# Optimization experiments

Hardware: AMD Instinct MI355X
Metric: run time of the kernel (lower is better)

## Reference

```python
import jax, jax.numpy as jnp
import numpy as np

POOL_NUM = 1024
NEIGHBOR_NUM = 16


def setup_inputs() -> dict:
    key = jax.random.key(0)
    k1, k2 = jax.random.split(key)
    vertices = jax.random.normal(k1, (8, 4096, 3), dtype=jnp.float32)
    feature_map = jax.random.normal(k2, (8, 4096, 256), dtype=jnp.float32)
    return {"vertices": vertices, "feature_map": feature_map}


def _get_neighbor_index(vertices, neighbor_num):
    # vertices: (bs, N, 3) -> neighbor_index: (bs, N, neighbor_num)
    inner = jnp.einsum('bnd,bmd->bnm', vertices, vertices)  # (bs, N, N)
    quadratic = jnp.sum(vertices ** 2, axis=2)              # (bs, N)
    distance = -2.0 * inner + quadratic[:, None, :] + quadratic[:, :, None]
    # smallest k+1 distances -> top_k on negated distance
    _, idx = jax.lax.top_k(-distance, neighbor_num + 1)     # (bs, N, k+1)
    return idx[:, :, 1:]                                    # drop self


def reference(vertices, feature_map):
    bs, vertice_num, _ = vertices.shape
    neighbor_index = _get_neighbor_index(vertices, NEIGHBOR_NUM)  # (bs, N, k)
    # gather neighbor features: (bs, N, k, C)
    id_0 = jnp.arange(bs)[:, None, None]
    neighbor_feature = feature_map[id_0, neighbor_index]
    pooled_feature = jnp.max(neighbor_feature, axis=2)            # (bs, N, C)
    # deterministic random subsample of vertices (torch uses randperm)
    sample_idx = jax.random.permutation(jax.random.key(42), vertice_num)[:POOL_NUM]
    vertices_pool = vertices[:, sample_idx, :]                    # (bs, P, 3)
    feature_map_pool = pooled_feature[:, sample_idx, :]           # (bs, P, C)
    return (vertices_pool, feature_map_pool)
```

## Files before the change

### kernel.cpp

```cpp
#include <hip/hip_runtime.h>
#include <stdint.h>
#include <string.h>
#include <algorithm>

#define NV 4096
#define NPOOL 1024
#define NB 8
#define KNB 16
#define REMOVED 0xFFFFFFFFu
#define HIDX(b) ((((b) >> 4) | (((b) & 15) << 6)))

struct SIdx { unsigned short v[NPOOL]; };

static inline void tf2x32_host(uint32_t k0, uint32_t k1,
                               uint32_t c0, uint32_t c1,
                               uint32_t& o0, uint32_t& o1) {
  uint32_t ks0 = k0, ks1 = k1, ks2 = k0 ^ k1 ^ 0x1BD11BDAu;
  uint32_t x0 = c0 + ks0, x1 = c1 + ks1;
#define TFR(r) { x0 += x1; x1 = (x1 << (r)) | (x1 >> (32 - (r))); x1 ^= x0; }
  TFR(13) TFR(15) TFR(26) TFR(6)
  x0 += ks1; x1 += ks2 + 1u;
  TFR(17) TFR(29) TFR(16) TFR(24)
  x0 += ks2; x1 += ks0 + 2u;
  TFR(13) TFR(15) TFR(26) TFR(6)
  x0 += ks0; x1 += ks1 + 3u;
  TFR(17) TFR(29) TFR(16) TFR(24)
  x0 += ks1; x1 += ks2 + 4u;
  TFR(13) TFR(15) TFR(26) TFR(6)
  x0 += ks2; x1 += ks0 + 5u;
#undef TFR
  o0 = x0; o1 = x1;
}

static void compute_sample_idx(SIdx& out) {
  static_assert(sizeof(SIdx) == 2048, "kernarg size");
  uint64_t arr[NV];
  uint16_t x[NV], tmp[NV];
  for (int i = 0; i < NV; ++i) x[i] = (uint16_t)i;
  uint32_t kh = 0u, kl = 42u;
  for (int round = 0; round < 2; ++round) {
    uint32_t nkh, nkl, sh, sl, t0, t1;
    tf2x32_host(kh, kl, 0u, 0u, nkh, nkl);
    tf2x32_host(kh, kl, 0u, 1u, sh, sl);
    kh = nkh; kl = nkl;
    for (int i = 0; i < NV; ++i) {
      tf2x32_host(sh, sl, 0u, (uint32_t)i, t0, t1);
      arr[i] = ((uint64_t)(t0 ^ t1) << 32) | (uint32_t)i;
    }
    std::sort(arr, arr + NV);
    for (int i = 0; i < NV; ++i) tmp[i] = x[(uint32_t)(arr[i] & 0xffffffffu)];
    memcpy(x, tmp, sizeof(x));
  }
  for (int i = 0; i < NPOOL; ++i) out.v[i] = x[i];
}

#define FALLBACK(D, TAUB, WIN)                                             \
  {                                                                        \
    uint32_t mask = 0;                                                     \
    for (int r = 0; r < KNB; ++r) {                                        \
      uint32_t bv = REMOVED, bm = 0xFFFFFFFFu;                             \
      _Pragma("unroll")                                                    \
      for (int t = 0; t < 16; ++t) {                                       \
        const uint32_t v = (((mask >> t) & 1u) || ((D[t] >> 22) > (TAUB))) \
                               ? REMOVED : D[t];                           \
        const uint32_t m = (uint32_t)((tid << 4) + t);                     \
        if (v < bv || (v == bv && m < bm)) { bv = v; bm = m; }             \
      }                                                                    \
      for (int off = 32; off > 0; off >>= 1) {                             \
        const uint32_t ov = (uint32_t)__shfl_down((int)bv, off);           \
        const uint32_t om = (uint32_t)__shfl_down((int)bm, off);           \
        if (ov < bv || (ov == bv && om < bm)) { bv = ov; bm = om; }        \
      }                                                                    \
      if (lane == 0) wmin[warp] = ((unsigned long long)bv << 32) | bm;     \
      __syncthreads();                                                     \
      const unsigned long long p0 = wmin[0], p1 = wmin[1];                 \
      const unsigned long long p2 = wmin[2], p3 = wmin[3];                 \
      const unsigned long long pa = (p0 < p1) ? p0 : p1;                   \
      const unsigned long long pb = (p2 < p3) ? p2 : p3;                   \
      const int w = (int)(((pa < pb) ? pa : pb) & 0xFFFFFFFFu);            \
      if (tid == 0) (WIN)[r] = w;                                          \
      if (tid == (w >> 4)) mask |= 1u << (w & 15);                         \
      __syncthreads();                                                     \
    }                                                                      \
  }

#define APPEND(D, TAUB, QI)                                                \
  _Pragma("unroll")                                                        \
  for (int t = 0; t < 16; ++t) {                                           \
    const uint32_t v = D[t];                                               \
    if ((v >> 22) <= (TAUB)) {                                             \
      const int s = atomicAdd(&s_nc[QI], 1);                               \
      if (s < 64)                                                          \
        cand[QI][s] =                                                      \
            ((unsigned long long)v << 32) | (uint32_t)((tid << 4) + t);    \
    }                                                                      \
  }

__global__ __launch_bounds__(256) void knn_pool_kernel(
    const float* __restrict__ vertices, const float* __restrict__ fm,
    const SIdx sidx,
    float* __restrict__ outV, float* __restrict__ outF) {
  __shared__ uint32_t hist[4][1024];
  __shared__ unsigned long long cand[4][64];
  __shared__ unsigned long long wmin[4];
  __shared__ int winners[4][KNB];
  __shared__ int s_nc[4], s_tb[4];

  const int tid = threadIdx.x;
  const int lane = tid & 63;
  const int warp = tid >> 6;
  const int blk = blockIdx.x;
  const int b = blk & 7;
  const int ibase = (blk >> 3) << 2;
  const int n0 = (int)sidx.v[ibase + 0];
  const int n1 = (int)sidx.v[ibase + 1];
  const int n2 = (int)sidx.v[ibase + 2];
  const int n3 = (int)sidx.v[ibase + 3];

  const float* vb = vertices + (size_t)b * NV * 3;
  const float q0x = vb[n0 * 3 + 0], q0y = vb[n0 * 3 + 1], q0z = vb[n0 * 3 + 2];
  const float q1x = vb[n1 * 3 + 0], q1y = vb[n1 * 3 + 1], q1z = vb[n1 * 3 + 2];
  const float q2x = vb[n2 * 3 + 0], q2y = vb[n2 * 3 + 1], q2z = vb[n2 * 3 + 2];
  const float q3x = vb[n3 * 3 + 0], q3y = vb[n3 * 3 + 1], q3z = vb[n3 * 3 + 2];
  const float qn0 = __fadd_rn(__fadd_rn(__fmul_rn(q0x, q0x), __fmul_rn(q0y, q0y)), __fmul_rn(q0z, q0z));
  const float qn1 = __fadd_rn(__fadd_rn(__fmul_rn(q1x, q1x), __fmul_rn(q1y, q1y)), __fmul_rn(q1z, q1z));
  const float qn2 = __fadd_rn(__fadd_rn(__fmul_rn(q2x, q2x), __fmul_rn(q2y, q2y)), __fmul_rn(q2z, q2z));
  const float qn3 = __fadd_rn(__fadd_rn(__fmul_rn(q3x, q3x), __fmul_rn(q3y, q3y)), __fmul_rn(q3z, q3z));

  const float4* vb4 = (const float4*)vb + tid * 12;
  float f[48];
#pragma unroll
  for (int j = 0; j < 12; ++j) {
    const float4 v4 = vb4[j];
    f[4 * j + 0] = v4.x; f[4 * j + 1] = v4.y;
    f[4 * j + 2] = v4.z; f[4 * j + 3] = v4.w;
  }

  uint32_t d0[16], d1[16], d2[16], d3[16];
#pragma unroll
  for (int t = 0; t < 16; ++t) {
    const int m = (tid << 4) + t;
    const float cx = f[3 * t + 0], cy = f[3 * t + 1], cz = f[3 * t + 2];
    const float qm = __fadd_rn(__fadd_rn(__fmul_rn(cx, cx), __fmul_rn(cy, cy)),
                               __fmul_rn(cz, cz));
    const float in0 = __fmaf_rn(cz, q0z, __fmaf_rn(cy, q0y, __fmul_rn(cx, q0x)));
    const float in1 = __fmaf_rn(cz, q1z, __fmaf_rn(cy, q1y, __fmul_rn(cx, q1x)));
    const float in2 = __fmaf_rn(cz, q2z, __fmaf_rn(cy, q2y, __fmul_rn(cx, q2x)));
    const float in3 = __fmaf_rn(cz, q3z, __fmaf_rn(cy, q3y, __fmul_rn(cx, q3x)));
    const float ds0 = __fadd_rn(__fadd_rn(__fmul_rn(-2.0f, in0), qm), qn0);
    const float ds1 = __fadd_rn(__fadd_rn(__fmul_rn(-2.0f, in1), qm), qn1);
    const float ds2 = __fadd_rn(__fadd_rn(__fmul_rn(-2.0f, in2), qm), qn2);
    const float ds3 = __fadd_rn(__fadd_rn(__fmul_rn(-2.0f, in3), qm), qn3);
    d0[t] = (m == n0) ? REMOVED : __float_as_uint(ds0);
    d1[t] = (m == n1) ? REMOVED : __float_as_uint(ds1);
    d2[t] = (m == n2) ? REMOVED : __float_as_uint(ds2);
    d3[t] = (m == n3) ? REMOVED : __float_as_uint(ds3);
  }

  uint32_t mn0 = d0[0], mn1 = d1[0], mn2 = d2[0], mn3 = d3[0];
#pragma unroll
  for (int t = 1; t < 16; ++t) {
    mn0 = (d0[t] < mn0) ? d0[t] : mn0;
    mn1 = (d1[t] < mn1) ? d1[t] : mn1;
    mn2 = (d2[t] < mn2) ? d2[t] : mn2;
    mn3 = (d3[t] < mn3) ? d3[t] : mn3;
  }

  {
    const uint4 z4 = make_uint4(0, 0, 0, 0);
    uint4* h4 = (uint4*)&hist[0][0];
    h4[tid] = z4; h4[tid + 256] = z4; h4[tid + 512] = z4; h4[tid + 768] = z4;
  }
  if (tid < 4) s_nc[tid] = 0;
  __syncthreads();

  atomicAdd(&hist[0][HIDX(mn0 >> 22)], 1u);
  atomicAdd(&hist[1][HIDX(mn1 >> 22)], 1u);
  atomicAdd(&hist[2][HIDX(mn2 >> 22)], 1u);
  atomicAdd(&hist[3][HIDX(mn3 >> 22)], 1u);
  __syncthreads();

  {
    const uint32_t* H = hist[warp];
    uint32_t s = 0;
#pragma unroll
    for (int j = 0; j < 16; ++j) s += H[j * 64 + lane];
    uint32_t inc = s;
    for (int off = 1; off < 64; off <<= 1) {
      const uint32_t o = (uint32_t)__shfl_up((int)inc, off);
      if (lane >= off) inc += o;
    }
    const uint32_t pre = inc - s;
    const bool cross = (pre < KNB) && (inc >= KNB);
    const unsigned long long bal = __ballot(cross);
    const int leader = __ffsll((unsigned long long)bal) - 1;
    if (lane == leader) {
      uint32_t c = pre;
      int tb = lane * 16 + 15;
      for (int j = 0; j < 16; ++j) {
        const uint32_t h = H[j * 64 + lane];
        if (c + h >= KNB) { tb = lane * 16 + j; break; }
        c += h;
      }
      s_tb[warp] = tb;
    }
  }
  __syncthreads();

  const uint32_t taub0 = (uint32_t)s_tb[0];
  const uint32_t taub1 = (uint32_t)s_tb[1];
  const uint32_t taub2 = (uint32_t)s_tb[2];
  const uint32_t taub3 = (uint32_t)s_tb[3];

  APPEND(d0, taub0, 0)
  APPEND(d1, taub1, 1)
  APPEND(d2, taub2, 2)
  APPEND(d3, taub3, 3)
  __syncthreads();

  const int C0 = s_nc[0], C1 = s_nc[1], C2 = s_nc[2], C3 = s_nc[3];
  {
    const int C = s_nc[warp];
    if (C <= 64) {
      const unsigned long long me =
          (lane < C) ? cand[warp][lane] : 0xFFFFFFFFFFFFFFFFull;
      int rank = 0;
      for (int j = 0; j < C; ++j) rank += (cand[warp][j] < me) ? 1 : 0;
      if (lane < C && rank < KNB) winners[warp][rank] = (int)(me & 0xFFFFFFFFu);
    }
  }
  __syncthreads();

  if (C0 > 64) FALLBACK(d0, taub0, winners[0]);
  if (C1 > 64) FALLBACK(d1, taub1, winners[1]);
  if (C2 > 64) FALLBACK(d2, taub2, winners[2]);
  if (C3 > 64) FALLBACK(d3, taub3, winners[3]);

  const float* fmb = fm + (size_t)b * NV * 256;
  {
    const int* W = winners[warp];
    const int ii = ibase + warp;
    float4 acc = make_float4(-INFINITY, -INFINITY, -INFINITY, -INFINITY);
#pragma unroll
    for (int s = 0; s < KNB; ++s) {
      const float4 v = ((const float4*)(fmb + (size_t)W[s] * 256))[lane];
      acc.x = fmaxf(acc.x, v.x); acc.y = fmaxf(acc.y, v.y);
      acc.z = fmaxf(acc.z, v.z); acc.w = fmaxf(acc.w, v.w);
    }
    ((float4*)(outF + ((size_t)b * NPOOL + ii) * 256))[lane] = acc;
    if (lane < 3) {
      const int nn = (warp == 0) ? n0 : (warp == 1) ? n1 : (warp == 2) ? n2 : n3;
      outV[((size_t)b * NPOOL + ii) * 3 + lane] = vb[nn * 3 + lane];
    }
  }
}

extern "C" void kernel_launch(void* const* d_in, const int* in_sizes, int n_in,
                              void* d_out, int out_size, void* d_ws, size_t ws_size,
                              hipStream_t stream) {
  const float* vertices = (const float*)d_in[0];
  const float* fm = (const float*)d_in[1];
  float* out = (float*)d_out;
  float* outV = out;
  float* outF = out + NB * NPOOL * 3;

  SIdx sidx;
  compute_sample_idx(sidx);

  knn_pool_kernel<<<NB * NPOOL / 4, 256, 0, stream>>>(vertices, fm, sidx, outV, outF);
}
```

Measured before the change: 42.84 us.

## Double block size to 512 threads, halving per-thread candidates and splitting gather

Each block now runs 512 threads, so every thread scores 8 candidate vertices instead of 16. This cuts register pressure and per-thread serial work. The threshold search in the histogram is now a parallel shuffle scan instead of a serial leader loop, and there is a fast path when exactly 16 candidates qualify. The feature gather splits the 16 neighbours across two warp halves and merges their partial maxima through shared memory. The cost is an extra block-wide sync, wider fallback reductions, and 8-warp blocks, which may lower occupancy flexibility.

Result: faster. 37.71 us (-12.0%).

```diff
diff --git a/kernel.cpp b/kernel.cpp
--- a/kernel.cpp
+++ b/kernel.cpp
@@ -54,16 +54,16 @@
   for (int i = 0; i < NPOOL; ++i) out.v[i] = x[i];
 }
 
-#define FALLBACK(D, TAUB, WIN)                                             \
+#define FALLBACK8(D, TAUB, WIN)                                            \
   {                                                                        \
     uint32_t mask = 0;                                                     \
     for (int r = 0; r < KNB; ++r) {                                        \
       uint32_t bv = REMOVED, bm = 0xFFFFFFFFu;                             \
       _Pragma("unroll")                                                    \
-      for (int t = 0; t < 16; ++t) {                                       \
+      for (int t = 0; t < 8; ++t) {                                        \
         const uint32_t v = (((mask >> t) & 1u) || ((D[t] >> 22) > (TAUB))) \
                                ? REMOVED : D[t];                           \
-        const uint32_t m = (uint32_t)((tid << 4) + t);                     \
+        const uint32_t m = (uint32_t)((tid << 3) + t);                     \
         if (v < bv || (v == bv && m < bm)) { bv = v; bm = m; }             \
       }                                                                    \
       for (int off = 32; off > 0; off >>= 1) {                             \
@@ -73,36 +73,24 @@
       }                                                                    \
       if (lane == 0) wmin[warp] = ((unsigned long long)bv << 32) | bm;     \
       __syncthreads();                                                     \
-      const unsigned long long p0 = wmin[0], p1 = wmin[1];                 \
-      const unsigned long long p2 = wmin[2], p3 = wmin[3];                 \
-      const unsigned long long pa = (p0 < p1) ? p0 : p1;                   \
-      const unsigned long long pb = (p2 < p3) ? p2 : p3;                   \
-      const int w = (int)(((pa < pb) ? pa : pb) & 0xFFFFFFFFu);            \
+      unsigned long long best = wmin[0];                                   \
+      _Pragma("unroll")                                                    \
+      for (int p = 1; p < 8; ++p) { const unsigned long long c = wmin[p];  \
+        if (c < best) best = c; }                                          \
+      const int w = (int)(best & 0xFFFFFFFFu);                             \
       if (tid == 0) (WIN)[r] = w;                                          \
-      if (tid == (w >> 4)) mask |= 1u << (w & 15);                         \
+      if (tid == (w >> 3)) mask |= 1u << (w & 7);                          \
       __syncthreads();                                                     \
     }                                                                      \
   }
 
-#define APPEND(D, TAUB, QI)                                                \
-  _Pragma("unroll")                                                        \
-  for (int t = 0; t < 16; ++t) {                                           \
-    const uint32_t v = D[t];                                               \
-    if ((v >> 22) <= (TAUB)) {                                             \
-      const int s = atomicAdd(&s_nc[QI], 1);                               \
-      if (s < 64)                                                          \
-        cand[QI][s] =                                                      \
-            ((unsigned long long)v << 32) | (uint32_t)((tid << 4) + t);    \
-    }                                                                      \
-  }
-
-__global__ __launch_bounds__(256) void knn_pool_kernel(
+__global__ __launch_bounds__(512) void knn_pool_kernel(
     const float* __restrict__ vertices, const float* __restrict__ fm,
     const SIdx sidx,
     float* __restrict__ outV, float* __restrict__ outF) {
-  __shared__ uint32_t hist[4][1024];
+  __shared__ __attribute__((aligned(16))) uint32_t hist[4][1024];
   __shared__ unsigned long long cand[4][64];
-  __shared__ unsigned long long wmin[4];
+  __shared__ unsigned long long wmin[8];
   __shared__ int winners[4][KNB];
   __shared__ int s_nc[4], s_tb[4];
 
@@ -117,6 +105,13 @@
   const int n2 = (int)sidx.v[ibase + 2];
   const int n3 = (int)sidx.v[ibase + 3];
 
+  {
+    const uint4 z4 = make_uint4(0, 0, 0, 0);
+    uint4* h4 = (uint4*)&hist[0][0];
+    h4[tid] = z4; h4[tid + 512] = z4;
+    if (tid < 4) s_nc[tid] = 0;
+  }
+
   const float* vb = vertices + (size_t)b * NV * 3;
   const float q0x = vb[n0 * 3 + 0], q0y = vb[n0 * 3 + 1], q0z = vb[n0 * 3 + 2];
   const float q1x = vb[n1 * 3 + 0], q1y = vb[n1 * 3 + 1], q1z = vb[n1 * 3 + 2];
@@ -127,19 +122,19 @@
   const float qn2 = __fadd_rn(__fadd_rn(__fmul_rn(q2x, q2x), __fmul_rn(q2y, q2y)), __fmul_rn(q2z, q2z));
   const float qn3 = __fadd_rn(__fadd_rn(__fmul_rn(q3x, q3x), __fmul_rn(q3y, q3y)), __fmul_rn(q3z, q3z));
 
-  const float4* vb4 = (const float4*)vb + tid * 12;
-  float f[48];
-#pragma unroll
-  for (int j = 0; j < 12; ++j) {
+  const float4* vb4 = (const float4*)vb + tid * 6;
+  float f[24];
+#pragma unroll
+  for (int j = 0; j < 6; ++j) {
     const float4 v4 = vb4[j];
     f[4 * j + 0] = v4.x; f[4 * j + 1] = v4.y;
     f[4 * j + 2] = v4.z; f[4 * j + 3] = v4.w;
   }
 
-  uint32_t d0[16], d1[16], d2[16], d3[16];
-#pragma unroll
-  for (int t = 0; t < 16; ++t) {
-    const int m = (tid << 4) + t;
+  uint32_t d0[8], d1[8], d2[8], d3[8];
+#pragma unroll
+  for (int t = 0; t < 8; ++t) {
+    const int m = (tid << 3) + t;
     const float cx = f[3 * t + 0], cy = f[3 * t + 1], cz = f[3 * t + 2];
     const float qm = __fadd_rn(__fadd_rn(__fmul_rn(cx, cx), __fmul_rn(cy, cy)),
                                __fmul_rn(cz, cz));
@@ -159,19 +154,12 @@
 
   uint32_t mn0 = d0[0], mn1 = d1[0], mn2 = d2[0], mn3 = d3[0];
 #pragma unroll
-  for (int t = 1; t < 16; ++t) {
+  for (int t = 1; t < 8; ++t) {
     mn0 = (d0[t] < mn0) ? d0[t] : mn0;
     mn1 = (d1[t] < mn1) ? d1[t] : mn1;
     mn2 = (d2[t] < mn2) ? d2[t] : mn2;
     mn3 = (d3[t] < mn3) ? d3[t] : mn3;
   }
-
-  {
-    const uint4 z4 = make_uint4(0, 0, 0, 0);
-    uint4* h4 = (uint4*)&hist[0][0];
-    h4[tid] = z4; h4[tid + 256] = z4; h4[tid + 512] = z4; h4[tid + 768] = z4;
-  }
-  if (tid < 4) s_nc[tid] = 0;
   __syncthreads();
 
   atomicAdd(&hist[0][HIDX(mn0 >> 22)], 1u);
@@ -180,7 +168,7 @@
   atomicAdd(&hist[3][HIDX(mn3 >> 22)], 1u);
   __syncthreads();
 
-  {
+  if (warp < 4) {
     const uint32_t* H = hist[warp];
     uint32_t s = 0;
 #pragma unroll
@@ -193,17 +181,19 @@
     const uint32_t pre = inc - s;
     const bool cross = (pre < KNB) && (inc >= KNB);
     const unsigned long long bal = __ballot(cross);
-    const int leader = __ffsll((unsigned long long)bal) - 1;
-    if (lane == leader) {
-      uint32_t c = pre;
-      int tb = lane * 16 + 15;
-      for (int j = 0; j < 16; ++j) {
-        const uint32_t h = H[j * 64 + lane];
-        if (c + h >= KNB) { tb = lane * 16 + j; break; }
-        c += h;
-      }
-      s_tb[warp] = tb;
-    }
+    const int g = __ffsll((unsigned long long)bal) - 1;
+    const uint32_t c0 = (uint32_t)__shfl((int)pre, g);
+    const uint32_t h = (lane < 16) ? H[lane * 64 + g] : 0u;
+    uint32_t hin = h;
+    for (int off = 1; off < 16; off <<= 1) {
+      const uint32_t o = (uint32_t)__shfl_up((int)hin, off);
+      if (lane >= off) hin += o;
+    }
+    const uint32_t incj = c0 + hin;
+    const bool crossj = (lane < 16) && ((incj - h) < KNB) && (incj >= KNB);
+    const unsigned long long bal2 = __ballot(crossj);
+    const int jstar = __ffsll((unsigned long long)bal2) - 1;
+    if (lane == 0) s_tb[warp] = g * 16 + jstar;
   }
   __syncthreads();
 
@@ -212,45 +202,80 @@
   const uint32_t taub2 = (uint32_t)s_tb[2];
   const uint32_t taub3 = (uint32_t)s_tb[3];
 
-  APPEND(d0, taub0, 0)
-  APPEND(d1, taub1, 1)
-  APPEND(d2, taub2, 2)
-  APPEND(d3, taub3, 3)
+#pragma unroll
+  for (int t = 0; t < 8; ++t) {
+    const uint32_t m = (uint32_t)((tid << 3) + t);
+    const uint32_t v0 = d0[t];
+    if ((v0 >> 22) <= taub0) {
+      const int s = atomicAdd(&s_nc[0], 1);
+      if (s < 64) cand[0][s] = ((unsigned long long)v0 << 32) | m;
+    }
+    const uint32_t v1 = d1[t];
+    if ((v1 >> 22) <= taub1) {
+      const int s = atomicAdd(&s_nc[1], 1);
+      if (s < 64) cand[1][s] = ((unsigned long long)v1 << 32) | m;
+    }
+    const uint32_t v2 = d2[t];
+    if ((v2 >> 22) <= taub2) {
+      const int s = atomicAdd(&s_nc[2], 1);
+      if (s < 64) cand[2][s] = ((unsigned long long)v2 << 32) | m;
+    }
+    const uint32_t v3 = d3[t];
+    if ((v3 >> 22) <= taub3) {
+      const int s = atomicAdd(&s_nc[3], 1);
+      if (s < 64) cand[3][s] = ((unsigned long long)v3 << 32) | m;
+    }
+  }
   __syncthreads();
 
   const int C0 = s_nc[0], C1 = s_nc[1], C2 = s_nc[2], C3 = s_nc[3];
-  {
+  if (warp < 4) {
     const int C = s_nc[warp];
     if (C <= 64) {
-      const unsigned long long me =
-          (lane < C) ? cand[warp][lane] : 0xFFFFFFFFFFFFFFFFull;
-      int rank = 0;
-      for (int j = 0; j < C; ++j) rank += (cand[warp][j] < me) ? 1 : 0;
-      if (lane < C && rank < KNB) winners[warp][rank] = (int)(me & 0xFFFFFFFFu);
-    }
-  }
-  __syncthreads();
-
-  if (C0 > 64) FALLBACK(d0, taub0, winners[0]);
-  if (C1 > 64) FALLBACK(d1, taub1, winners[1]);
-  if (C2 > 64) FALLBACK(d2, taub2, winners[2]);
-  if (C3 > 64) FALLBACK(d3, taub3, winners[3]);
+      if (C == KNB) {
+        if (lane < KNB) winners[warp][lane] = (int)(cand[warp][lane] & 0xFFFFFFFFu);
+      } else {
+        const unsigned long long me =
+            (lane < C) ? cand[warp][lane] : 0xFFFFFFFFFFFFFFFFull;
+        int rank = 0;
+        for (int j = 0; j < C; ++j) rank += (cand[warp][j] < me) ? 1 : 0;
+        if (lane < C && rank < KNB) winners[warp][rank] = (int)(me & 0xFFFFFFFFu);
+      }
+    }
+  }
+  __syncthreads();
+
+  if (C0 > 64) FALLBACK8(d0, taub0, winners[0]);
+  if (C1 > 64) FALLBACK8(d1, taub1, winners[1]);
+  if (C2 > 64) FALLBACK8(d2, taub2, winners[2]);
+  if (C3 > 64) FALLBACK8(d3, taub3, winners[3]);
 
   const float* fmb = fm + (size_t)b * NV * 256;
   {
-    const int* W = winners[warp];
-    const int ii = ibase + warp;
+    const int q = warp & 3;
+    const int half = warp >> 2;
+    const int* W = winners[q];
     float4 acc = make_float4(-INFINITY, -INFINITY, -INFINITY, -INFINITY);
 #pragma unroll
-    for (int s = 0; s < KNB; ++s) {
-      const float4 v = ((const float4*)(fmb + (size_t)W[s] * 256))[lane];
+    for (int s = 0; s < 8; ++s) {
+      const float4 v = ((const float4*)(fmb + (size_t)W[half * 8 + s] * 256))[lane];
       acc.x = fmaxf(acc.x, v.x); acc.y = fmaxf(acc.y, v.y);
       acc.z = fmaxf(acc.z, v.z); acc.w = fmaxf(acc.w, v.w);
     }
-    ((float4*)(outF + ((size_t)b * NPOOL + ii) * 256))[lane] = acc;
-    if (lane < 3) {
-      const int nn = (warp == 0) ? n0 : (warp == 1) ? n1 : (warp == 2) ? n2 : n3;
-      outV[((size_t)b * NPOOL + ii) * 3 + lane] = vb[nn * 3 + lane];
+    float4* part = (float4*)&hist[0][0];
+    if (half == 1) {
+      part[q * 64 + lane] = acc;
+      if (lane < 3) {
+        const int nq = (q == 0) ? n0 : (q == 1) ? n1 : (q == 2) ? n2 : n3;
+        outV[((size_t)b * NPOOL + ibase + q) * 3 + lane] = vb[nq * 3 + lane];
+      }
+    }
+    __syncthreads();
+    if (half == 0) {
+      const float4 o = part[q * 64 + lane];
+      acc.x = fmaxf(acc.x, o.x); acc.y = fmaxf(acc.y, o.y);
+      acc.z = fmaxf(acc.z, o.z); acc.w = fmaxf(acc.w, o.w);
+      ((float4*)(outF + ((size_t)b * NPOOL + ibase + q) * 256))[lane] = acc;
     }
   }
 }
@@ -267,5 +292,5 @@
   SIdx sidx;
   compute_sample_idx(sidx);
 
-  knn_pool_kernel<<<NB * NPOOL / 4, 256, 0, stream>>>(vertices, fm, sidx, outV, outF);
-}
+  knn_pool_kernel<<<NB * NPOOL / 4, 512, 0, stream>>>(vertices, fm, sidx, outV, outF);
+}
```
